# Kernel optimization log

Hardware: AMD Instinct MI355X
Metric: run time of the kernel (lower is better)

## Reference

```python
import jax, jax.numpy as jnp
import numpy as np

B, S, D, H = 2, 2048, 1024, 16
DEPTH = D // H


def setup_inputs() -> dict:
    key = jax.random.key(0)
    ks = jax.random.split(key, 10)
    batch = jax.random.normal(ks[0], (B, S, D), dtype=jnp.float32)
    # variable-length valid rows, like padded batches in the original repo
    lengths = jax.random.randint(ks[1], (B,), S // 2, S + 1)
    mask = jnp.arange(S)[None, :] < lengths[:, None]  # (B, S) bool
    scale = 1.0 / np.sqrt(D)
    Wq = jax.random.normal(ks[2], (D, D), dtype=jnp.float32) * scale
    bq = jnp.zeros((D,), dtype=jnp.float32)
    Wk = jax.random.normal(ks[3], (D, D), dtype=jnp.float32) * scale
    bk = jnp.zeros((D,), dtype=jnp.float32)
    Wv = jax.random.normal(ks[4], (D, D), dtype=jnp.float32) * scale
    bv = jnp.zeros((D,), dtype=jnp.float32)
    Wo = jax.random.normal(ks[5], (D, D), dtype=jnp.float32) * scale
    bo = jnp.zeros((D,), dtype=jnp.float32)
    return {"batch": batch, "mask": mask, "Wq": Wq, "bq": bq, "Wk": Wk,
            "bk": bk, "Wv": Wv, "bv": bv, "Wo": Wo, "bo": bo}


def _split_heads(x):
    # (B, S, D) -> (B, H, S, depth)
    b, s, _ = x.shape
    return x.reshape(b, s, H, DEPTH).transpose(0, 2, 1, 3)


def reference(batch, mask, Wq, bq, Wk, bk, Wv, bv, Wo, bo):
    b, s, _ = batch.shape
    Q = _split_heads(batch @ Wq + bq)
    K = _split_heads(batch @ Wk + bk)
    V = _split_heads(batch @ Wv + bv)
    # scaled dot-product attention with key-padding mask
    logits = jnp.einsum('bhqd,bhkd->bhqk', Q, K) / jnp.sqrt(
        jnp.asarray(DEPTH, dtype=batch.dtype))
    neg = (~mask).astype(batch.dtype) * -1e9  # (B, S)
    logits = logits + neg[:, None, None, :]
    attn = jax.nn.softmax(logits, axis=-1)
    X = jnp.einsum('bhqk,bhkd->bhqd', attn, V)
    X = X.transpose(0, 2, 1, 3).reshape(b, s, D)
    return X @ Wo + bo
```

## Files before the change

kernel.cpp:

```cpp
#include <hip/hip_runtime.h>
#include <hip/hip_bf16.h>

#define DEV __device__ __forceinline__

typedef short bf16x8 __attribute__((ext_vector_type(8)));
typedef float f32x4  __attribute__((ext_vector_type(4)));
typedef float f32x16 __attribute__((ext_vector_type(16)));

#define Bc 2
#define Sc 2048
#define Dc 1024
#define Hc 16

#define OFF_XB    0u
#define OFF_WQKVT 8388608u
#define OFF_WOT   14680064u
#define OFF_Q     16777216u
#define OFF_K     25165824u
#define OFF_VT    33554432u
#define OFF_XA    41943040u
#define OFF_BIASC 50331648u
#define OFF_LENS  50343936u

DEV short f2bf(float f) {
    __hip_bfloat16 h = __float2bfloat16(f);
    union { __hip_bfloat16 h; short s; } u; u.h = h; return u.s;
}

DEV int cvtpk(float lo, float hi_) {
    int r;
    asm("v_cvt_pk_bf16_f32 %0, %1, %2" : "=v"(r) : "v"(lo), "v"(hi_));
    return r;
}

DEV void gload16(const void* g, void* l) {
    __builtin_amdgcn_global_load_lds((const __attribute__((address_space(1))) void*)g,
                                     (__attribute__((address_space(3))) void*)l, 16, 0, 0);
}

union I4BF { int i[4]; bf16x8 v; };

DEV bf16x8 vread(const char* Vc, int row, int kkbyte, int hi8, int rsw) {
    union { short4 h[2]; bf16x8 v; } u;
    u.h[0] = *(const short4*)(Vc + row * 128 + ((kkbyte + hi8) ^ rsw));
    u.h[1] = *(const short4*)(Vc + row * 128 + ((kkbyte + 16 + hi8) ^ rsw));
    return u.v;
}


__global__ void cast_bf16_kernel(const float* __restrict__ in, short* __restrict__ out, int n4) {
    int i = blockIdx.x * blockDim.x + threadIdx.x;
    if (i >= n4) return;
    float4 v = ((const float4*)in)[i];
    short4 o;
    o.x = f2bf(v.x); o.y = f2bf(v.y); o.z = f2bf(v.z); o.w = f2bf(v.w);
    ((short4*)out)[i] = o;
}

__global__ void wtrans_kernel(const float* __restrict__ Wq, const float* __restrict__ Wk,
                              const float* __restrict__ Wv, const float* __restrict__ Wo,
                              short* __restrict__ WQKVT, short* __restrict__ WOT) {
    const float* src; short* dst;
    int z = blockIdx.z;
    if (z == 0)      { src = Wq; dst = WQKVT; }
    else if (z == 1) { src = Wk; dst = WQKVT + 1024 * 1024; }
    else if (z == 2) { src = Wv; dst = WQKVT + 2 * 1024 * 1024; }
    else             { src = Wo; dst = WOT; }
    __shared__ float t[32][33];
    int tx = threadIdx.x, ty = threadIdx.y;
    int r0 = blockIdx.y * 32, c0 = blockIdx.x * 32;
#pragma unroll
    for (int i = 0; i < 4; i++)
        t[ty + i * 8][tx] = src[(size_t)(r0 + ty + i * 8) * Dc + c0 + tx];
    __syncthreads();
#pragma unroll
    for (int i = 0; i < 4; i++)
        dst[(size_t)(c0 + ty + i * 8) * Dc + r0 + tx] = f2bf(t[tx][ty + i * 8]);
}

__global__ void prep_small_kernel(const float* __restrict__ bq, const float* __restrict__ bk,
                                  const float* __restrict__ bv,
                                  const unsigned char* __restrict__ mask,
                                  float* __restrict__ biasc, int* __restrict__ lens) {
    int blk = blockIdx.x, t = threadIdx.x;
    if (blk == 0) {
        if (t < Dc) { biasc[t] = bq[t]; biasc[Dc + t] = bk[t]; biasc[2 * Dc + t] = bv[t]; }
        return;
    }
    int b = blk - 1;
    bool is_i32 = (mask[1] == 0);
    __shared__ int cnt;
    if (t == 0) cnt = 0;
    __syncthreads();
    int local = 0;
    for (int s = t; s < Sc; s += blockDim.x) {
        bool v = is_i32 ? (((const int*)mask)[b * Sc + s] != 0) : (mask[b * Sc + s] != 0);
        local += v ? 1 : 0;
    }
    atomicAdd(&cnt, local);
    __syncthreads();
    if (t == 0) lens[b] = cnt;
}

__global__ __launch_bounds__(256) void vtrans_kernel(const short* __restrict__ V,
                                                     short* __restrict__ VT) {
    __shared__ short t[64][65];
    int tid = threadIdx.x;
    int bh = blockIdx.y, s0 = blockIdx.x * 64;
    int rr = tid >> 2, c4 = (tid & 3) * 16;
    const short* vrow = V + ((size_t)bh * Sc + s0 + rr) * 64 + c4;
    *(bf16x8*)&t[rr][c4]     = *(const bf16x8*)(vrow);
    *(bf16x8*)&t[rr][c4 + 8] = *(const bf16x8*)(vrow + 8);
    __syncthreads();
    bf16x8 a, b2;
#pragma unroll
    for (int i = 0; i < 8; i++) { a[i] = t[c4 + i][rr]; b2[i] = t[c4 + 8 + i][rr]; }
    short* orow = VT + ((size_t)bh * 64 + rr) * Sc + s0 + c4;
    *(bf16x8*)(orow)     = a;
    *(bf16x8*)(orow + 8) = b2;
}

__global__ __launch_bounds__(256) void gemm_qkv_kernel(
    const short* __restrict__ A, const short* __restrict__ BT, const float* __restrict__ bias,
    short* __restrict__ Qp, short* __restrict__ Kp, short* __restrict__ Vp)
{
    __shared__ short As[128 * 32];
    __shared__ short Bs[128 * 32];
    int tid = threadIdx.x, lane = tid & 63, wave = tid >> 6;
    int l15 = lane & 15, lhi = lane >> 4;
    int bm = blockIdx.x, bn = blockIdx.y;
    int wm = wave >> 1, wn = wave & 1;

    const f32x4 fzero = {0.f, 0.f, 0.f, 0.f};
    f32x4 acc[4][4];
#pragma unroll
    for (int i = 0; i < 4; i++)
#pragma unroll
        for (int j = 0; j < 4; j++) acc[i][j] = fzero;

    const char* Ab = (const char*)A;
    const char* Bb = (const char*)BT;

    for (int k0 = 0; k0 < 1024; k0 += 32) {
#pragma unroll
        for (int i = 0; i < 2; i++) {
            int o = wave * 2048 + i * 1024 + lane * 16;
            int row = o >> 6, cb = o & 63;
            gload16(Ab + ((size_t)(bm * 128 + row) * 1024 + k0) * 2 + cb,
                    (char*)As + wave * 2048 + i * 1024);
            gload16(Bb + ((size_t)(bn * 128 + row) * 1024 + k0) * 2 + cb,
                    (char*)Bs + wave * 2048 + i * 1024);
        }
        __syncthreads();
        bf16x8 af[4], bfv[4];
#pragma unroll
        for (int i = 0; i < 4; i++) {
            af[i]  = *(const bf16x8*)(As + (wm * 64 + i * 16 + l15) * 32 + lhi * 8);
            bfv[i] = *(const bf16x8*)(Bs + (wn * 64 + i * 16 + l15) * 32 + lhi * 8);
        }
#pragma unroll
        for (int i = 0; i < 4; i++)
#pragma unroll
            for (int j = 0; j < 4; j++)
                acc[i][j] = __builtin_amdgcn_mfma_f32_16x16x32_bf16(af[i], bfv[j], acc[i][j], 0, 0, 0);
        __syncthreads();
    }

#pragma unroll
    for (int i = 0; i < 4; i++)
#pragma unroll
        for (int j = 0; j < 4; j++) {
            int c = bn * 128 + wn * 64 + j * 16 + l15;
            float bc = bias[c];
            int rb = bm * 128 + wm * 64 + i * 16 + 4 * lhi;
#pragma unroll
            for (int reg = 0; reg < 4; reg++) {
                int r = rb + reg;
                float v = acc[i][j][reg] + bc;
                int which = c >> 10, cc = c & 1023, h = cc >> 6, d = cc & 63;
                int b = r >> 11, s = r & 2047;
                int bh = b * Hc + h;
                if (which == 0) v *= 0.18033688f;
                short sv = f2bf(v);
                size_t idx = ((size_t)bh * Sc + s) * 64 + d;
                if (which == 0)      Qp[idx] = sv;
                else if (which == 1) Kp[idx] = sv;
                else                 Vp[idx] = sv;
            }
        }
}

__global__ __launch_bounds__(256) void gemm_out_kernel(
    const short* __restrict__ A, const short* __restrict__ BT, const float* __restrict__ bias,
    float* __restrict__ outF)
{
    __shared__ short As[128 * 32];
    __shared__ short Bs[64 * 32];
    int tid = threadIdx.x, lane = tid & 63, wave = tid >> 6;
    int l15 = lane & 15, lhi = lane >> 4;
    int bm = blockIdx.x, bn = blockIdx.y;

    const f32x4 fzero = {0.f, 0.f, 0.f, 0.f};
    f32x4 acc[2][4];
#pragma unroll
    for (int i = 0; i < 2; i++)
#pragma unroll
        for (int j = 0; j < 4; j++) acc[i][j] = fzero;

    const char* Ab = (const char*)A;
    const char* Bb = (const char*)BT;

    for (int k0 = 0; k0 < 1024; k0 += 32) {
#pragma unroll
        for (int i = 0; i < 2; i++) {
            int o = wave * 2048 + i * 1024 + lane * 16;
            int row = o >> 6, cb = o & 63;
            gload16(Ab + ((size_t)(bm * 128 + row) * 1024 + k0) * 2 + cb,
                    (char*)As + wave * 2048 + i * 1024);
        }
        {
            int o = wave * 1024 + lane * 16;
            int row = o >> 6, cb = o & 63;
            gload16(Bb + ((size_t)(bn * 64 + row) * 1024 + k0) * 2 + cb,
                    (char*)Bs + wave * 1024);
        }
        __syncthreads();
        bf16x8 af[2], bfv[4];
#pragma unroll
        for (int i = 0; i < 2; i++)
            af[i] = *(const bf16x8*)(As + (wave * 32 + i * 16 + l15) * 32 + lhi * 8);
#pragma unroll
        for (int j = 0; j < 4; j++)
            bfv[j] = *(const bf16x8*)(Bs + (j * 16 + l15) * 32 + lhi * 8);
#pragma unroll
        for (int i = 0; i < 2; i++)
#pragma unroll
            for (int j = 0; j < 4; j++)
                acc[i][j] = __builtin_amdgcn_mfma_f32_16x16x32_bf16(af[i], bfv[j], acc[i][j], 0, 0, 0);
        __syncthreads();
    }

#pragma unroll
    for (int i = 0; i < 2; i++)
#pragma unroll
        for (int j = 0; j < 4; j++) {
            int c = bn * 64 + j * 16 + l15;
            float bc = bias[c];
            int rb = bm * 128 + wave * 32 + i * 16 + 4 * lhi;
#pragma unroll
            for (int reg = 0; reg < 4; reg++)
                outF[(size_t)(rb + reg) * Dc + c] = acc[i][j][reg] + bc;
        }
}

__global__ __launch_bounds__(256) void attn_kernel(
    const short* __restrict__ Qp, const short* __restrict__ Kp, const short* __restrict__ VTp,
    const int* __restrict__ lens, short* __restrict__ Xout)
{
    int tid = threadIdx.x, lane = tid & 63, wave = tid >> 6;
    int l31 = lane & 31, hi = lane >> 5;

    int orig = blockIdx.x;
    int swz = (orig & 7) * 64 + (orig >> 3);
    int bx = swz & 15, bh = swz >> 4;
    int b = bh >> 4, h = bh & 15;
    int q0 = bx * 128 + wave * 32;

    __shared__ short Kt[2][64 * 64];
    __shared__ short Vt[2][64 * 64];

    const short* Qb  = Qp + (size_t)bh * Sc * 64;
    const char*  Kb  = (const char*)(Kp + (size_t)bh * Sc * 64);
    const char*  VTb = (const char*)(VTp + (size_t)bh * 64 * Sc);

    bf16x8 qf[4];
#pragma unroll
    for (int kk = 0; kk < 4; kk++)
        qf[kk] = *(const bf16x8*)(Qb + (size_t)(q0 + l31) * 64 + kk * 16 + hi * 8);

    f32x16 xacc0, xacc1;
#pragma unroll
    for (int r = 0; r < 16; r++) { xacc0[r] = 0.f; xacc1[r] = 0.f; }
    float lreg = 0.f;

    int len = lens[b];
    int nt = (len + 63) >> 6;
    int rsw = (l31 & 7) << 4;
    int hi8 = hi * 8;

#define STAGE(bufi, kt_)                                                              \
    {                                                                                 \
        int k0_ = (kt_) * 64;                                                         \
        _Pragma("unroll")                                                             \
        for (int i = 0; i < 2; i++) {                                                 \
            int o = wave * 2048 + i * 1024 + lane * 16;                               \
            int row = o >> 7, cb = o & 127;                                           \
            int scb = cb ^ ((row & 7) << 4);                                          \
            gload16(Kb + (size_t)(k0_ + row) * 128 + scb,                             \
                    (char*)&Kt[bufi][0] + wave * 2048 + i * 1024);                    \
            gload16(VTb + (size_t)row * (Sc * 2) + (size_t)k0_ * 2 + scb,             \
                    (char*)&Vt[bufi][0] + wave * 2048 + i * 1024);                    \
        }                                                                             \
    }

#define DOHALF(Kc, Vc, ROFF, KBASE, KT)                                               \
    {                                                                                 \
        f32x16 s;                                                                     \
        _Pragma("unroll")                                                             \
        for (int r = 0; r < 16; r++) s[r] = 0.f;                                      \
        __builtin_amdgcn_s_setprio(1);                                                \
        _Pragma("unroll")                                                             \
        for (int kk = 0; kk < 4; kk++) {                                              \
            bf16x8 kf = *(const bf16x8*)((Kc) + (ROFF + l31) * 128 +                  \
                                         ((kk * 32 + hi * 16) ^ rsw));                \
            s = __builtin_amdgcn_mfma_f32_32x32x16_bf16(kf, qf[kk], s, 0, 0, 0);      \
        }                                                                             \
        __builtin_amdgcn_s_setprio(0);                                                \
        if ((KT) == nt - 1) {                                                         \
            int rem = len - (KT) * 64;                                                \
            if (rem < (KBASE) + 32) {                                                 \
                _Pragma("unroll")                                                     \
                for (int r = 0; r < 16; r++) {                                        \
                    int key0 = (KBASE) + 4 * hi + (r & 3) + 8 * (r >> 2);             \
                    if (key0 >= rem) s[r] = -3.0e38f;                                 \
                }                                                                     \
            }                                                                         \
        }                                                                             \
        _Pragma("unroll")                                                             \
        for (int r = 0; r < 16; r++) { s[r] = exp2f(s[r]); lreg += s[r]; }            \
        I4BF u, w;                                                                    \
        u.i[0] = cvtpk(s[0], s[1]);   u.i[1] = cvtpk(s[2], s[3]);                     \
        u.i[2] = cvtpk(s[4], s[5]);   u.i[3] = cvtpk(s[6], s[7]);                     \
        w.i[0] = cvtpk(s[8], s[9]);   w.i[1] = cvtpk(s[10], s[11]);                   \
        w.i[2] = cvtpk(s[12], s[13]); w.i[3] = cvtpk(s[14], s[15]);                   \
        __builtin_amdgcn_s_setprio(1);                                                \
        {                                                                             \
            bf16x8 v0 = vread((Vc), l31,      (KBASE) * 2,      hi8, rsw);            \
            bf16x8 v1 = vread((Vc), 32 + l31, (KBASE) * 2,      hi8, rsw);            \
            xacc0 = __builtin_amdgcn_mfma_f32_32x32x16_bf16(v0, u.v, xacc0, 0, 0, 0); \
            xacc1 = __builtin_amdgcn_mfma_f32_32x32x16_bf16(v1, u.v, xacc1, 0, 0, 0); \
            bf16x8 v2 = vread((Vc), l31,      (KBASE) * 2 + 32, hi8, rsw);            \
            bf16x8 v3 = vread((Vc), 32 + l31, (KBASE) * 2 + 32, hi8, rsw);            \
            xacc0 = __builtin_amdgcn_mfma_f32_32x32x16_bf16(v2, w.v, xacc0, 0, 0, 0); \
            xacc1 = __builtin_amdgcn_mfma_f32_32x32x16_bf16(v3, w.v, xacc1, 0, 0, 0); \
        }                                                                             \
        __builtin_amdgcn_s_setprio(0);                                                \
    }

#define DOTILE(BUFI, KT)                                                              \
    {                                                                                 \
        const char* Kc_ = (const char*)&Kt[BUFI][0];                                  \
        const char* Vc_ = (const char*)&Vt[BUFI][0];                                  \
        DOHALF(Kc_, Vc_, 0, 0, KT);                                                   \
        DOHALF(Kc_, Vc_, 32, 32, KT);                                                 \
    }

    STAGE(0, 0);
    __syncthreads();

    int kt = 0;
    while (kt + 2 <= nt) {
        if (kt + 1 < nt) STAGE(1, kt + 1);
        DOTILE(0, kt);
        __syncthreads();
        if (kt + 2 < nt) STAGE(0, kt + 2);
        DOTILE(1, kt + 1);
        __syncthreads();
        kt += 2;
    }
    if (kt < nt) DOTILE(0, kt);

    float lfull = lreg + __shfl_xor(lreg, 32, 64);
    float rl = 1.0f / lfull;
    short* orow = Xout + (size_t)(b * Sc + q0 + l31) * Dc + h * 64;
#pragma unroll
    for (int g = 0; g < 4; g++) {
        short4 o;
        o.x = f2bf(xacc0[4 * g + 0] * rl);
        o.y = f2bf(xacc0[4 * g + 1] * rl);
        o.z = f2bf(xacc0[4 * g + 2] * rl);
        o.w = f2bf(xacc0[4 * g + 3] * rl);
        *(short4*)(orow + 4 * hi + 8 * g) = o;
    }
#pragma unroll
    for (int g = 0; g < 4; g++) {
        short4 o;
        o.x = f2bf(xacc1[4 * g + 0] * rl);
        o.y = f2bf(xacc1[4 * g + 1] * rl);
        o.z = f2bf(xacc1[4 * g + 2] * rl);
        o.w = f2bf(xacc1[4 * g + 3] * rl);
        *(short4*)(orow + 32 + 4 * hi + 8 * g) = o;
    }
}


extern "C" void kernel_launch(void* const* d_in, const int* in_sizes, int n_in,
                              void* d_out, int out_size, void* d_ws, size_t ws_size,
                              hipStream_t stream) {
    const float* batch = (const float*)d_in[0];
    const unsigned char* mask = (const unsigned char*)d_in[1];
    const float* Wq = (const float*)d_in[2];
    const float* bq = (const float*)d_in[3];
    const float* Wk = (const float*)d_in[4];
    const float* bk = (const float*)d_in[5];
    const float* Wv = (const float*)d_in[6];
    const float* bv = (const float*)d_in[7];
    const float* Wo = (const float*)d_in[8];
    const float* bo = (const float*)d_in[9];

    char* ws = (char*)d_ws;
    short* XB    = (short*)(ws + OFF_XB);
    short* WQKVT = (short*)(ws + OFF_WQKVT);
    short* WOT   = (short*)(ws + OFF_WOT);
    short* Qb    = (short*)(ws + OFF_Q);
    short* Kb    = (short*)(ws + OFF_K);
    short* VTb   = (short*)(ws + OFF_VT);
    short* XAb   = (short*)(ws + OFF_XA);
    float* BIASC = (float*)(ws + OFF_BIASC);
    int*   LENS  = (int*)(ws + OFF_LENS);
    short* Vscr  = (short*)d_out;

    cast_bf16_kernel<<<4096, 256, 0, stream>>>(batch, XB, 1048576);
    wtrans_kernel<<<dim3(32, 32, 4), dim3(32, 8), 0, stream>>>(Wq, Wk, Wv, Wo, WQKVT, WOT);
    prep_small_kernel<<<3, 1024, 0, stream>>>(bq, bk, bv, mask, BIASC, LENS);

    gemm_qkv_kernel<<<dim3(32, 24), 256, 0, stream>>>(XB, WQKVT, BIASC, Qb, Kb, Vscr);
    vtrans_kernel<<<dim3(32, 32), 256, 0, stream>>>(Vscr, VTb);
    attn_kernel<<<512, 256, 0, stream>>>(Qb, Kb, VTb, LENS, XAb);
    gemm_out_kernel<<<dim3(32, 16), 256, 0, stream>>>(XAb, WOT, bo, (float*)d_out);
}
```

Baseline: 140.2 us.

## Fuse V transpose into QKV GEMM epilogue and remap attention blocks per XCD

The QKV GEMM blocks that produce V now stage their tile in shared memory transposed and write V^T directly with vector stores, so the separate vtrans kernel and its scratch round trip are gone. The attention kernel's block-to-(batch, head) mapping is changed so each XCD handles the same two heads from both batches, aiming for better L2 reuse of K/V. This costs extra shared memory in the GEMM (about 34KB more), which may lower occupancy.

```diff
diff --git a/kernel.cpp b/kernel.cpp
--- a/kernel.cpp
+++ b/kernel.cpp
@@ -102,30 +102,13 @@
     if (t == 0) lens[b] = cnt;
 }
 
-__global__ __launch_bounds__(256) void vtrans_kernel(const short* __restrict__ V,
-                                                     short* __restrict__ VT) {
-    __shared__ short t[64][65];
-    int tid = threadIdx.x;
-    int bh = blockIdx.y, s0 = blockIdx.x * 64;
-    int rr = tid >> 2, c4 = (tid & 3) * 16;
-    const short* vrow = V + ((size_t)bh * Sc + s0 + rr) * 64 + c4;
-    *(bf16x8*)&t[rr][c4]     = *(const bf16x8*)(vrow);
-    *(bf16x8*)&t[rr][c4 + 8] = *(const bf16x8*)(vrow + 8);
-    __syncthreads();
-    bf16x8 a, b2;
-#pragma unroll
-    for (int i = 0; i < 8; i++) { a[i] = t[c4 + i][rr]; b2[i] = t[c4 + 8 + i][rr]; }
-    short* orow = VT + ((size_t)bh * 64 + rr) * Sc + s0 + c4;
-    *(bf16x8*)(orow)     = a;
-    *(bf16x8*)(orow + 8) = b2;
-}
-
 __global__ __launch_bounds__(256) void gemm_qkv_kernel(
     const short* __restrict__ A, const short* __restrict__ BT, const float* __restrict__ bias,
-    short* __restrict__ Qp, short* __restrict__ Kp, short* __restrict__ Vp)
+    short* __restrict__ Qp, short* __restrict__ Kp, short* __restrict__ VTp)
 {
     __shared__ short As[128 * 32];
     __shared__ short Bs[128 * 32];
+    __shared__ short Vt2[2][64][136];
     int tid = threadIdx.x, lane = tid & 63, wave = tid >> 6;
     int l15 = lane & 15, lhi = lane >> 4;
     int bm = blockIdx.x, bn = blockIdx.y;
@@ -166,28 +149,55 @@
         __syncthreads();
     }
 
-#pragma unroll
-    for (int i = 0; i < 4; i++)
-#pragma unroll
-        for (int j = 0; j < 4; j++) {
-            int c = bn * 128 + wn * 64 + j * 16 + l15;
-            float bc = bias[c];
-            int rb = bm * 128 + wm * 64 + i * 16 + 4 * lhi;
-#pragma unroll
-            for (int reg = 0; reg < 4; reg++) {
-                int r = rb + reg;
-                float v = acc[i][j][reg] + bc;
-                int which = c >> 10, cc = c & 1023, h = cc >> 6, d = cc & 63;
-                int b = r >> 11, s = r & 2047;
-                int bh = b * Hc + h;
-                if (which == 0) v *= 0.18033688f;
-                short sv = f2bf(v);
-                size_t idx = ((size_t)bh * Sc + s) * 64 + d;
-                if (which == 0)      Qp[idx] = sv;
-                else if (which == 1) Kp[idx] = sv;
-                else                 Vp[idx] = sv;
+    if (bn < 16) {
+#pragma unroll
+        for (int i = 0; i < 4; i++)
+#pragma unroll
+            for (int j = 0; j < 4; j++) {
+                int c = bn * 128 + wn * 64 + j * 16 + l15;
+                float bc = bias[c];
+                int rb = bm * 128 + wm * 64 + i * 16 + 4 * lhi;
+#pragma unroll
+                for (int reg = 0; reg < 4; reg++) {
+                    int r = rb + reg;
+                    float v = acc[i][j][reg] + bc;
+                    int which = c >> 10, cc = c & 1023, h = cc >> 6, d = cc & 63;
+                    int b = r >> 11, s = r & 2047;
+                    int bh = b * Hc + h;
+                    if (which == 0) v *= 0.18033688f;
+                    short sv = f2bf(v);
+                    size_t idx = ((size_t)bh * Sc + s) * 64 + d;
+                    if (which == 0) Qp[idx] = sv;
+                    else            Kp[idx] = sv;
+                }
             }
-        }
+    } else {
+#pragma unroll
+        for (int i = 0; i < 4; i++)
+#pragma unroll
+            for (int j = 0; j < 4; j++) {
+                int c = bn * 128 + wn * 64 + j * 16 + l15;
+                float bc = bias[c];
+                int d = c & 63;
+                int swb = wm * 64 + i * 16 + 4 * lhi;
+                short4 pk;
+                pk.x = f2bf(acc[i][j][0] + bc);
+                pk.y = f2bf(acc[i][j][1] + bc);
+                pk.z = f2bf(acc[i][j][2] + bc);
+                pk.w = f2bf(acc[i][j][3] + bc);
+                *(short4*)&Vt2[wn][d][swb] = pk;
+            }
+        __syncthreads();
+        int u = tid;
+        int tilei = u >> 7, rowd = (u >> 1) & 63, halfs = u & 1;
+        int h = (bn - 16) * 2 + tilei;
+        int b0 = bm >> 4, s0 = (bm & 15) * 128;
+        short* orow = VTp + ((size_t)(b0 * Hc + h) * 64 + rowd) * Sc + s0 + halfs * 64;
+        const short* lrow = &Vt2[tilei][rowd][halfs * 64];
+#pragma unroll
+        for (int k = 0; k < 8; k++)
+            *(bf16x8*)(orow + k * 8) = *(const bf16x8*)(lrow + k * 8);
+    }
 }
 
 __global__ __launch_bounds__(256) void gemm_out_kernel(
@@ -261,8 +271,9 @@
     int l31 = lane & 31, hi = lane >> 5;
 
     int orig = blockIdx.x;
-    int swz = (orig & 7) * 64 + (orig >> 3);
-    int bx = swz & 15, bh = swz >> 4;
+    int xcd = orig & 7, idx = orig >> 3;
+    int j = idx & 3, bx = idx >> 2;
+    int bh = ((j >> 1) << 4) + xcd * 2 + (j & 1);
     int b = bh >> 4, h = bh & 15;
     int q0 = bx * 128 + wave * 32;
 
@@ -418,14 +429,12 @@
     short* XAb   = (short*)(ws + OFF_XA);
     float* BIASC = (float*)(ws + OFF_BIASC);
     int*   LENS  = (int*)(ws + OFF_LENS);
-    short* Vscr  = (short*)d_out;
 
     cast_bf16_kernel<<<4096, 256, 0, stream>>>(batch, XB, 1048576);
     wtrans_kernel<<<dim3(32, 32, 4), dim3(32, 8), 0, stream>>>(Wq, Wk, Wv, Wo, WQKVT, WOT);
     prep_small_kernel<<<3, 1024, 0, stream>>>(bq, bk, bv, mask, BIASC, LENS);
 
-    gemm_qkv_kernel<<<dim3(32, 24), 256, 0, stream>>>(XB, WQKVT, BIASC, Qb, Kb, Vscr);
-    vtrans_kernel<<<dim3(32, 32), 256, 0, stream>>>(Vscr, VTb);
+    gemm_qkv_kernel<<<dim3(32, 24), 256, 0, stream>>>(XB, WQKVT, BIASC, Qb, Kb, VTb);
     attn_kernel<<<512, 256, 0, stream>>>(Qb, Kb, VTb, LENS, XAb);
     gemm_out_kernel<<<dim3(32, 16), 256, 0, stream>>>(XAb, WOT, bo, (float*)d_out);
 }
```

After: 150.3 us. +7.2%, slower.
